# Optimization experiments

Hardware: AMD Instinct MI355X
Metric: run time of the kernel (lower is better)

The kernel has to match this reference:

```python
import jax, jax.numpy as jnp
import numpy as np

N_LOC = 20000
N_EXP = 200000
H = 64
E = 1500000
L = 400000


def setup_inputs() -> dict:
    key = jax.random.key(0)
    ks = jax.random.split(key, 24)
    f = jnp.float32
    w = lambda k, shp: jax.random.normal(k, shp, dtype=f) * 0.1
    # edges: ('location','of','experts'): src in [0,N_LOC), dst in [0,N_EXP)
    src = jax.random.randint(ks[0], (E,), 0, N_LOC)
    dst = jax.random.randint(ks[1], (E,), 0, N_EXP)
    edge_of = jnp.stack([src, dst])          # location -> experts
    edge_rev = jnp.stack([dst, src])         # experts -> location (ToUndirected)
    row = jax.random.randint(ks[2], (L,), 0, N_LOC)
    col = jax.random.randint(ks[3], (L,), 0, N_EXP)
    edge_label_index = jnp.stack([row, col])
    return dict(
        emb_loc=w(ks[4], (N_LOC, H)), emb_exp=w(ks[5], (N_EXP, H)),
        W1l_of=w(ks[6], (H, H)), b1_of=jnp.zeros((H,), f), W1r_of=w(ks[7], (H, H)),
        W1l_rev=w(ks[8], (H, H)), b1_rev=jnp.zeros((H,), f), W1r_rev=w(ks[9], (H, H)),
        W2l_of=w(ks[10], (H, H)), b2_of=jnp.zeros((H,), f), W2r_of=w(ks[11], (H, H)),
        W2l_rev=w(ks[12], (H, H)), b2_rev=jnp.zeros((H,), f), W2r_rev=w(ks[13], (H, H)),
        dW1=w(ks[14], (2 * H, H)), db1=jnp.zeros((H,), f),
        dW2=w(ks[15], (H, 1)), db2=jnp.zeros((1,), f),
        edge_of=edge_of, edge_rev=edge_rev, edge_label_index=edge_label_index,
    )


def _sage(x_src, x_dst, edge, Wl, b, Wr, n_dst):
    # PyG SAGEConv: lin_l(mean of neighbor msgs) + lin_r(x_dst); bias only in lin_l
    s, d = edge[0], edge[1]
    msg = x_src[s]                                   # [E, H] gather
    summed = jax.ops.segment_sum(msg, d, num_segments=n_dst)
    cnt = jax.ops.segment_sum(jnp.ones((edge.shape[1],), x_src.dtype), d, num_segments=n_dst)
    agg = summed / jnp.maximum(cnt, 1.0)[:, None]
    return agg @ Wl + b + x_dst @ Wr


def reference(emb_loc, emb_exp,
              W1l_of, b1_of, W1r_of, W1l_rev, b1_rev, W1r_rev,
              W2l_of, b2_of, W2r_of, W2l_rev, b2_rev, W2r_rev,
              dW1, db1, dW2, db2,
              edge_of, edge_rev, edge_label_index):
    # layer 1 (to_hetero: one conv per edge type; each dst type has one incoming type)
    z_exp = jax.nn.relu(_sage(emb_loc, emb_exp, edge_of, W1l_of, b1_of, W1r_of, N_EXP))
    z_loc = jax.nn.relu(_sage(emb_exp, emb_loc, edge_rev, W1l_rev, b1_rev, W1r_rev, N_LOC))
    # layer 2 (no relu)
    z_exp2 = _sage(z_loc, z_exp, edge_of, W2l_of, b2_of, W2r_of, N_EXP)
    z_loc2 = _sage(z_exp, z_loc, edge_rev, W2l_rev, b2_rev, W2r_rev, N_LOC)
    # EdgeDecoder: gather-concat-MLP
    row, col = edge_label_index[0], edge_label_index[1]
    z = jnp.concatenate([z_loc2[row], z_exp2[col]], axis=-1)  # [L, 2H]
    h = jax.nn.relu(z @ dW1 + db1)
    out = (h @ dW2 + db2).reshape(-1)
    return out
```

## Files before the change

kernel.cpp:

```cpp
#include <hip/hip_runtime.h>

#define H 64
#define NE 1500000
#define NLOC 20000
#define NEXP 200000
#define NL 400000
#define PAD_E 32
#define PAD_L 128
#define EPT 8
#define FILL_CHUNK 2048
#define NCHUNK ((NE + FILL_CHUNK - 1) / FILL_CHUNK)
#define FILL_BLOCKS (NCHUNK * 8)
#define DENSE1_BLOCKS 1280
#define PREP_BLOCKS (5 + DENSE1_BLOCKS + FILL_BLOCKS)

#define WS_NEED 90546112ULL

typedef int vint4 __attribute__((ext_vector_type(4)));
typedef _Float16 f16x8 __attribute__((ext_vector_type(8)));
typedef float f32x4 __attribute__((ext_vector_type(4)));

__device__ __forceinline__ float bcastf(float v, int k) {
  return __int_as_float(__builtin_amdgcn_readlane(__float_as_int(v), k));
}
__device__ __forceinline__ int bcasti(int v, int k) {
  return __builtin_amdgcn_readlane(v, k);
}

__global__ __launch_bounds__(256, 4) void prep_kernel(
    const int* __restrict__ src, const int* __restrict__ dst,
    int* __restrict__ cnt_loc, int* __restrict__ cnt_exp,
    int* __restrict__ nbr_loc, unsigned short* __restrict__ nbr_exp,
    const float* __restrict__ W2r_of, const float* __restrict__ W2l_of,
    const float* __restrict__ W2l_rev, const float* __restrict__ W2r_rev,
    const float* __restrict__ dW1, const float* __restrict__ b2_of,
    const float* __restrict__ b2_rev,
    float* __restrict__ Wf_q, float* __restrict__ Wf_y2,
    float* __restrict__ Wf_t2, float* __restrict__ Wf_p,
    float* __restrict__ bf_q, float* __restrict__ bf_p,
    const float* __restrict__ emb_loc, _Float16* __restrict__ Ylh,
    const float* __restrict__ W1l_of)
{
  const int lane = threadIdx.x & 63;
  if (blockIdx.x < 5) {
    const int w = threadIdx.x >> 6;
    const float* dW1a = dW1;
    const float* dW1b = dW1 + H * H;
    if (blockIdx.x < 4) {
      const float* A; const float* B; float* C;
      switch (blockIdx.x) {
        case 0:  A = W2r_of;  B = dW1b; C = Wf_q;  break;
        case 1:  A = W2l_of;  B = dW1b; C = Wf_y2; break;
        case 2:  A = W2l_rev; B = dW1a; C = Wf_t2; break;
        default: A = W2r_rev; B = dW1a; C = Wf_p;  break;
      }
      float b[H];
#pragma unroll
      for (int k = 0; k < H; k++) b[k] = B[k * H + lane];
      for (int r = w * 16; r < w * 16 + 16; r++) {
        const float xv = A[r * H + lane];
        float a0 = 0.f, a1 = 0.f;
#pragma unroll
        for (int k = 0; k < H; k += 2) {
          a0 += bcastf(xv, k)     * b[k];
          a1 += bcastf(xv, k + 1) * b[k + 1];
        }
        C[r * H + lane] = a0 + a1;
      }
    } else if (w < 2) {
      const float* bv_src = (w == 0) ? b2_of : b2_rev;
      const float* B      = (w == 0) ? dW1b  : dW1a;
      float* o            = (w == 0) ? bf_q  : bf_p;
      float wk[H];
#pragma unroll
      for (int k = 0; k < H; k++) wk[k] = B[k * H + lane];
      const float bv = bv_src[lane];
      float a = 0.f;
#pragma unroll
      for (int k = 0; k < H; k++) a += bcastf(bv, k) * wk[k];
      o[lane] = a;
    }
  } else if (blockIdx.x < 5 + DENSE1_BLOCKS) {
    const int vb = blockIdx.x - 5;
    const int gw = (vb * 256 + threadIdx.x) >> 6;
    const int nw = (DENSE1_BLOCKS * 256) >> 6;
    float w[H];
#pragma unroll
    for (int k = 0; k < H; k++) w[k] = W1l_of[k * H + lane];
    for (int i = gw; i < NLOC; i += nw) {
      const float xv = emb_loc[i * H + lane];
      float a0 = 0.f, a1 = 0.f;
#pragma unroll
      for (int k = 0; k < H; k += 2) {
        a0 += bcastf(xv, k)     * w[k];
        a1 += bcastf(xv, k + 1) * w[k + 1];
      }
      Ylh[i * H + lane] = (_Float16)(a0 + a1);
    }
  } else {
    const int fb = blockIdx.x - (5 + DENSE1_BLOCKS);
    const int p = fb & 7;
    const int chunk = fb >> 3;
    const long base = (long)chunk * FILL_CHUNK + threadIdx.x * EPT;
    if (base >= NE) return;
    vint4 s0 = __builtin_nontemporal_load((const vint4*)(src + base));
    vint4 s1 = __builtin_nontemporal_load((const vint4*)(src + base + 4));
    vint4 d0 = __builtin_nontemporal_load((const vint4*)(dst + base));
    vint4 d1 = __builtin_nontemporal_load((const vint4*)(dst + base + 4));
    int ss[EPT] = {s0.x, s0.y, s0.z, s0.w, s1.x, s1.y, s1.z, s1.w};
    int dd[EPT] = {d0.x, d0.y, d0.z, d0.w, d1.x, d1.y, d1.z, d1.w};
    const int elo = p * (NEXP / 8), ehi = elo + NEXP / 8;
    const int llo = p * (NLOC / 8), lhi = llo + NLOC / 8;
#pragma unroll
    for (int k = 0; k < EPT; k++) {
      const int d = dd[k];
      if (d >= elo && d < ehi) {
        int pos = atomicAdd(&cnt_exp[d], 1);
        if (pos < PAD_E) nbr_exp[d * PAD_E + pos] = (unsigned short)ss[k];
      }
    }
#pragma unroll
    for (int k = 0; k < EPT; k++) {
      const int s = ss[k];
      if (s >= llo && s < lhi) {
        int pos = atomicAdd(&cnt_loc[s], 1);
        if (pos < PAD_L) nbr_loc[s * PAD_L + pos] = dd[k];
      }
    }
  }
}

__global__ __launch_bounds__(256, 4) void mfma_pass_kernel(
    const unsigned short* __restrict__ nbr, const int* __restrict__ cnt,
    const _Float16* __restrict__ y,
    const float* a32, const _Float16* a16,
    _Float16* out1, const float* __restrict__ W1,
    const float* __restrict__ bias, int relu,
    _Float16* out2, const float* __restrict__ W2)
{
  const int w = threadIdx.x >> 6;
  const int lane = threadIdx.x & 63;
  const int q = lane >> 4;
  const int cidx = lane & 15;
  const int rb = blockIdx.x * 16;

  __shared__ float Gs[16 * H];

  f16x8 b1lo, b1hi, b2lo, b2hi;
#pragma unroll
  for (int j = 0; j < 8; j++) {
    b1lo[j] = (_Float16)W1[(q * 8 + j) * H + w * 16 + cidx];
    b1hi[j] = (_Float16)W1[(32 + q * 8 + j) * H + w * 16 + cidx];
  }
  if (out2) {
#pragma unroll
    for (int j = 0; j < 8; j++) {
      b2lo[j] = (_Float16)W2[(q * 8 + j) * H + w * 16 + cidx];
      b2hi[j] = (_Float16)W2[(32 + q * 8 + j) * H + w * 16 + cidx];
    }
  }

  if (y) {
    for (int rr = 0; rr < 4; rr++) {
      const int i = rb + w * 4 + rr;
      const int c = cnt[i];
      const int cc = min(c, PAD_E);
      const unsigned short* nb = nbr + (long)i * PAD_E;
      float s0 = 0.f, s1 = 0.f, s2 = 0.f, s3 = 0.f;
      const int id = (lane < cc) ? (int)nb[lane] : 0;
      int k = 0;
      const int m4 = cc & ~3;
      for (; k < m4; k += 4) {
        const int i0 = bcasti(id, k), i1 = bcasti(id, k + 1),
                  i2 = bcasti(id, k + 2), i3 = bcasti(id, k + 3);
        s0 += (float)y[(long)i0 * H + lane];
        s1 += (float)y[(long)i1 * H + lane];
        s2 += (float)y[(long)i2 * H + lane];
        s3 += (float)y[(long)i3 * H + lane];
      }
      for (; k < cc; k++) s0 += (float)y[(long)bcasti(id, k) * H + lane];
      Gs[(w * 4 + rr) * H + lane] =
          ((s0 + s1) + (s2 + s3)) / fmaxf((float)c, 1.0f);
    }
  }

  f16x8 a0, a1;
  if (a16) {
    const _Float16* ar = a16 + (long)(rb + cidx) * H;
    a0 = *(const f16x8*)(ar + q * 8);
    a1 = *(const f16x8*)(ar + 32 + q * 8);
  } else {
    const float* ar = a32 + (long)(rb + cidx) * H;
#pragma unroll
    for (int j = 0; j < 8; j++) {
      a0[j] = (_Float16)ar[q * 8 + j];
      a1[j] = (_Float16)ar[32 + q * 8 + j];
    }
  }
  f32x4 acc1 = {0.f, 0.f, 0.f, 0.f};
  acc1 = __builtin_amdgcn_mfma_f32_16x16x32_f16(a0, b1lo, acc1, 0, 0, 0);
  acc1 = __builtin_amdgcn_mfma_f32_16x16x32_f16(a1, b1hi, acc1, 0, 0, 0);
  f32x4 acc2 = {0.f, 0.f, 0.f, 0.f};
  if (out2) {
    acc2 = __builtin_amdgcn_mfma_f32_16x16x32_f16(a0, b2lo, acc2, 0, 0, 0);
    acc2 = __builtin_amdgcn_mfma_f32_16x16x32_f16(a1, b2hi, acc2, 0, 0, 0);
  }

  const float bj = bias ? bias[w * 16 + cidx] : 0.f;
  __syncthreads();
#pragma unroll
  for (int reg = 0; reg < 4; reg++) {
    const int r = q * 4 + reg;
    float v = acc1[reg] + bj;
    if (y) v += Gs[r * H + w * 16 + cidx];
    if (relu) v = fmaxf(v, 0.f);
    out1[(long)(rb + r) * H + w * 16 + cidx] = (_Float16)v;
    if (out2)
      out2[(long)(rb + r) * H + w * 16 + cidx] = (_Float16)acc2[reg];
  }
}

__global__ __launch_bounds__(256, 3) void loc_gather_fused_kernel(
    const int* __restrict__ nbr, const int* __restrict__ cnt,
    const _Float16* __restrict__ T, const float* __restrict__ x,
    float* __restrict__ zout, _Float16* __restrict__ y2out,
    const float* __restrict__ Wr, const float* __restrict__ bias,
    const float* __restrict__ Wfy2, int n)
{
  const int lane = threadIdx.x & 63;
  const int gw = (blockIdx.x * 256 + threadIdx.x) >> 6;
  const int nw = (gridDim.x * 256) >> 6;
  float wr[H], wy[H];
#pragma unroll
  for (int k = 0; k < H; k++) {
    wr[k] = Wr[k * H + lane];
    wy[k] = Wfy2[k * H + lane];
  }
  const float bj = bias[lane];
  for (int i = gw; i < n; i += nw) {
    const int c = cnt[i];
    const int cc = min(c, PAD_L);
    const int* nb = nbr + (long)i * PAD_L;
    float s0 = 0.f, s1 = 0.f, s2 = 0.f, s3 = 0.f;
    int e = 0;
    while (e < cc) {
      const int m = min(cc - e, 64);
      const int id = (lane < m) ? nb[e + lane] : 0;
      int k = 0;
      const int m4 = m & ~3;
      for (; k < m4; k += 4) {
        const int i0 = bcasti(id, k), i1 = bcasti(id, k + 1),
                  i2 = bcasti(id, k + 2), i3 = bcasti(id, k + 3);
        s0 += (float)T[(long)i0 * H + lane];
        s1 += (float)T[(long)i1 * H + lane];
        s2 += (float)T[(long)i2 * H + lane];
        s3 += (float)T[(long)i3 * H + lane];
      }
      for (; k < m; k++) s0 += (float)T[(long)bcasti(id, k) * H + lane];
      e += m;
    }
    const float agg = ((s0 + s1) + (s2 + s3)) / fmaxf((float)c, 1.0f);
    const float xv = x[i * H + lane];
    float a0 = 0.f, a1 = 0.f;
#pragma unroll
    for (int k = 0; k < H; k += 2) {
      a0 += bcastf(xv, k)     * wr[k];
      a1 += bcastf(xv, k + 1) * wr[k + 1];
    }
    const float z = fmaxf(agg + bj + a0 + a1, 0.0f);
    zout[i * H + lane] = z;
    float y0 = 0.f, y1 = 0.f;
#pragma unroll
    for (int k = 0; k < H; k += 2) {
      y0 += bcastf(z, k)     * wy[k];
      y1 += bcastf(z, k + 1) * wy[k + 1];
    }
    y2out[i * H + lane] = (_Float16)(y0 + y1);
  }
}

__global__ __launch_bounds__(256, 4) void loc_gather_kernel(
    const int* __restrict__ nbr, const int* __restrict__ cnt,
    const _Float16* __restrict__ T, const float* __restrict__ x,
    _Float16* __restrict__ out16,
    const float* __restrict__ Wr, const float* __restrict__ bias, int n)
{
  const int lane = threadIdx.x & 63;
  const int gw = (blockIdx.x * 256 + threadIdx.x) >> 6;
  const int nw = (gridDim.x * 256) >> 6;
  float wr[H];
#pragma unroll
  for (int k = 0; k < H; k++) wr[k] = Wr[k * H + lane];
  const float bj = bias[lane];
  for (int i = gw; i < n; i += nw) {
    const int c = cnt[i];
    const int cc = min(c, PAD_L);
    const int* nb = nbr + (long)i * PAD_L;
    float s0 = 0.f, s1 = 0.f, s2 = 0.f, s3 = 0.f;
    int e = 0;
    while (e < cc) {
      const int m = min(cc - e, 64);
      const int id = (lane < m) ? nb[e + lane] : 0;
      int k = 0;
      const int m4 = m & ~3;
      for (; k < m4; k += 4) {
        const int i0 = bcasti(id, k), i1 = bcasti(id, k + 1),
                  i2 = bcasti(id, k + 2), i3 = bcasti(id, k + 3);
        s0 += (float)T[(long)i0 * H + lane];
        s1 += (float)T[(long)i1 * H + lane];
        s2 += (float)T[(long)i2 * H + lane];
        s3 += (float)T[(long)i3 * H + lane];
      }
      for (; k < m; k++) s0 += (float)T[(long)bcasti(id, k) * H + lane];
      e += m;
    }
    const float agg = ((s0 + s1) + (s2 + s3)) / fmaxf((float)c, 1.0f);
    const float xv = x[i * H + lane];
    float a0 = 0.f, a1 = 0.f;
#pragma unroll
    for (int k = 0; k < H; k += 2) {
      a0 += bcastf(xv, k)     * wr[k];
      a1 += bcastf(xv, k + 1) * wr[k + 1];
    }
    out16[i * H + lane] = (_Float16)(agg + bj + a0 + a1);
  }
}

__global__ __launch_bounds__(256, 4) void edge_kernel(
    const int* __restrict__ row, const int* __restrict__ col,
    const _Float16* __restrict__ P, const _Float16* __restrict__ Q,
    const float* __restrict__ db1, const float* __restrict__ dW2,
    const float* __restrict__ db2, float* __restrict__ out)
{
  const int lane = threadIdx.x & 63;
  const int gw = (blockIdx.x * 256 + threadIdx.x) >> 6;
  const int nw = (gridDim.x * 256) >> 6;
  const float bj = db1[lane];
  const float w2 = dW2[lane];
  const float b2 = db2[0];
  for (int e = gw * 4; e < NL; e += nw * 4) {
    const int n4 = min(NL - e, 4);
    float h[4];
#pragma unroll
    for (int k = 0; k < 4; k++) {
      if (k < n4) {
        const int r = row[e + k], c = col[e + k];
        const float p = (float)P[(long)r * H + lane];
        const float q = (float)Q[(long)c * H + lane];
        h[k] = fmaxf(p + q + bj, 0.0f) * w2;
      } else h[k] = 0.f;
    }
#pragma unroll
    for (int off = 1; off < 64; off <<= 1) {
#pragma unroll
      for (int k = 0; k < 4; k++) h[k] += __shfl_xor(h[k], off);
    }
    if (lane == 0) {
#pragma unroll
      for (int k = 0; k < 4; k++)
        if (k < n4) out[e + k] = h[k] + b2;
    }
  }
}

extern "C" void kernel_launch(void* const* d_in, const int* in_sizes, int n_in,
                              void* d_out, int out_size, void* d_ws, size_t ws_size,
                              hipStream_t stream) {
  const float* emb_loc = (const float*)d_in[0];
  const float* emb_exp = (const float*)d_in[1];
  const float* W1l_of  = (const float*)d_in[2];
  const float* b1_of   = (const float*)d_in[3];
  const float* W1r_of  = (const float*)d_in[4];
  const float* W1l_rev = (const float*)d_in[5];
  const float* b1_rev  = (const float*)d_in[6];
  const float* W1r_rev = (const float*)d_in[7];
  const float* W2l_of  = (const float*)d_in[8];
  const float* b2_of   = (const float*)d_in[9];
  const float* W2r_of  = (const float*)d_in[10];
  const float* W2l_rev = (const float*)d_in[11];
  const float* b2_rev  = (const float*)d_in[12];
  const float* W2r_rev = (const float*)d_in[13];
  const float* dW1     = (const float*)d_in[14];
  const float* db1     = (const float*)d_in[15];
  const float* dW2     = (const float*)d_in[16];
  const float* db2     = (const float*)d_in[17];
  const int*   edge_of = (const int*)d_in[18];
  const int*   eli     = (const int*)d_in[20];

  const int* src = edge_of;
  const int* dst = edge_of + NE;
  const int* row = eli;
  const int* col = eli + NL;

  if (ws_size < WS_NEED) return;

  char* ws = (char*)d_ws;
  int*            cnt_loc = (int*)(ws);
  int*            cnt_exp = (int*)(ws + 80000);
  int*            nbr_loc = (int*)(ws + 880064);
  unsigned short* nbr_exp = (unsigned short*)(ws + 11120064);
  _Float16*       Ylh     = (_Float16*)(ws + 23920064);
  _Float16*       Y2fh    = (_Float16*)(ws + 26480064);
  float*          z_loc   = (float*)(ws + 29040064);
  _Float16*       PH      = (_Float16*)(ws + 34160064);
  _Float16*       ZE      = (_Float16*)(ws + 39280064);
  _Float16*       TH      = (_Float16*)(ws + 64880064);
  float*          Wf_q    = (float*)(ws + 90480064);
  float*          Wf_y2   = (float*)(ws + 90496448);
  float*          Wf_t2   = (float*)(ws + 90512832);
  float*          Wf_p    = (float*)(ws + 90529216);
  float*          bf_q    = (float*)(ws + 90545600);
  float*          bf_p    = (float*)(ws + 90545856);
  float*          out     = (float*)d_out;

  (void)hipMemsetAsync(ws, 0, 880000, stream);
  prep_kernel<<<PREP_BLOCKS, 256, 0, stream>>>(
      src, dst, cnt_loc, cnt_exp, nbr_loc, nbr_exp,
      W2r_of, W2l_of, W2l_rev, W2r_rev, dW1, b2_of, b2_rev,
      Wf_q, Wf_y2, Wf_t2, Wf_p, bf_q, bf_p,
      emb_loc, Ylh, W1l_of);

  mfma_pass_kernel<<<NEXP / 16, 256, 0, stream>>>(nbr_exp, cnt_exp, Ylh,
      emb_exp, (const _Float16*)nullptr, ZE, W1r_of, b1_of, 1, TH, W1l_rev);

  loc_gather_fused_kernel<<<1250, 256, 0, stream>>>(nbr_loc, cnt_loc, TH,
      emb_loc, z_loc, Y2fh, W1r_rev, b1_rev, Wf_y2, NLOC);

  mfma_pass_kernel<<<NEXP / 16, 256, 0, stream>>>(nbr_exp, cnt_exp, Y2fh,
      (const float*)nullptr, ZE, ZE, Wf_q, bf_q, 0, TH, Wf_t2);

  loc_gather_kernel<<<1250, 256, 0, stream>>>(nbr_loc, cnt_loc, TH,
      z_loc, PH, Wf_p, bf_p, NLOC);

  edge_kernel<<<2048, 256, 0, stream>>>(row, col, PH, ZE,
                                        db1, dW2, db2, out);
}
```

Measured before the change: 613.8 us.

## Restructure passes: compute z_exp projections in first pass, merge final gathers

The first expert pass now computes the relu'd z_exp tile, stages it in shared memory, and immediately applies the folded Wf_q and Wf_t2 projections. This removes the need to store and reread ZE in a second dense pass. The second expert pass becomes a gather-only update of PQ, and it is merged with the location gather into one launch using a block-range split. Folded weights now live in the output buffer as scratch, since edge_kernel overwrites it later, and the first pass uses more registers with launch bounds lowered to 3.

```diff
diff --git a/kernel.cpp b/kernel.cpp
--- a/kernel.cpp
+++ b/kernel.cpp
@@ -13,8 +13,10 @@
 #define FILL_BLOCKS (NCHUNK * 8)
 #define DENSE1_BLOCKS 1280
 #define PREP_BLOCKS (5 + DENSE1_BLOCKS + FILL_BLOCKS)
-
-#define WS_NEED 90546112ULL
+#define QFIN_BLOCKS 4096
+#define LOC2_BLOCKS 1250
+
+#define WS_NEED 113520000ULL
 
 typedef int vint4 __attribute__((ext_vector_type(4)));
 typedef _Float16 f16x8 __attribute__((ext_vector_type(8)));
@@ -34,10 +36,7 @@
     const float* __restrict__ W2r_of, const float* __restrict__ W2l_of,
     const float* __restrict__ W2l_rev, const float* __restrict__ W2r_rev,
     const float* __restrict__ dW1, const float* __restrict__ b2_of,
-    const float* __restrict__ b2_rev,
-    float* __restrict__ Wf_q, float* __restrict__ Wf_y2,
-    float* __restrict__ Wf_t2, float* __restrict__ Wf_p,
-    float* __restrict__ bf_q, float* __restrict__ bf_p,
+    const float* __restrict__ b2_rev, float* __restrict__ fold,
     const float* __restrict__ emb_loc, _Float16* __restrict__ Ylh,
     const float* __restrict__ W1l_of)
 {
@@ -49,10 +48,10 @@
     if (blockIdx.x < 4) {
       const float* A; const float* B; float* C;
       switch (blockIdx.x) {
-        case 0:  A = W2r_of;  B = dW1b; C = Wf_q;  break;
-        case 1:  A = W2l_of;  B = dW1b; C = Wf_y2; break;
-        case 2:  A = W2l_rev; B = dW1a; C = Wf_t2; break;
-        default: A = W2r_rev; B = dW1a; C = Wf_p;  break;
+        case 0:  A = W2r_of;  B = dW1b; C = fold;         break;
+        case 1:  A = W2l_of;  B = dW1b; C = fold + 4096;  break;
+        case 2:  A = W2l_rev; B = dW1a; C = fold + 8192;  break;
+        default: A = W2r_rev; B = dW1a; C = fold + 12288; break;
       }
       float b[H];
 #pragma unroll
@@ -70,7 +69,7 @@
     } else if (w < 2) {
       const float* bv_src = (w == 0) ? b2_of : b2_rev;
       const float* B      = (w == 0) ? dW1b  : dW1a;
-      float* o            = (w == 0) ? bf_q  : bf_p;
+      float* o            = (w == 0) ? fold + 16384 : fold + 16448;
       float wk[H];
 #pragma unroll
       for (int k = 0; k < H; k++) wk[k] = B[k * H + lane];
@@ -130,93 +129,106 @@
   }
 }
 
-__global__ __launch_bounds__(256, 4) void mfma_pass_kernel(
+__global__ __launch_bounds__(256, 3) void passA_kernel(
     const unsigned short* __restrict__ nbr, const int* __restrict__ cnt,
-    const _Float16* __restrict__ y,
-    const float* a32, const _Float16* a16,
-    _Float16* out1, const float* __restrict__ W1,
-    const float* __restrict__ bias, int relu,
-    _Float16* out2, const float* __restrict__ W2)
+    const _Float16* __restrict__ y, const float* __restrict__ x,
+    const float* __restrict__ W1r_of, const float* __restrict__ b1_of,
+    const float* __restrict__ W1l_rev,
+    const float* __restrict__ Wf_q, const float* __restrict__ Wf_t2,
+    _Float16* __restrict__ T1h, _Float16* __restrict__ PQ,
+    _Float16* __restrict__ T2h)
 {
   const int w = threadIdx.x >> 6;
   const int lane = threadIdx.x & 63;
   const int q = lane >> 4;
   const int cidx = lane & 15;
   const int rb = blockIdx.x * 16;
+  const int col = w * 16 + cidx;
 
   __shared__ float Gs[16 * H];
-
-  f16x8 b1lo, b1hi, b2lo, b2hi;
+  __shared__ float Zs[16][H + 1];
+
+  f16x8 bz0, bz1, bt0, bt1;
 #pragma unroll
   for (int j = 0; j < 8; j++) {
-    b1lo[j] = (_Float16)W1[(q * 8 + j) * H + w * 16 + cidx];
-    b1hi[j] = (_Float16)W1[(32 + q * 8 + j) * H + w * 16 + cidx];
-  }
-  if (out2) {
-#pragma unroll
-    for (int j = 0; j < 8; j++) {
-      b2lo[j] = (_Float16)W2[(q * 8 + j) * H + w * 16 + cidx];
-      b2hi[j] = (_Float16)W2[(32 + q * 8 + j) * H + w * 16 + cidx];
-    }
-  }
-
-  if (y) {
-    for (int rr = 0; rr < 4; rr++) {
-      const int i = rb + w * 4 + rr;
-      const int c = cnt[i];
-      const int cc = min(c, PAD_E);
-      const unsigned short* nb = nbr + (long)i * PAD_E;
-      float s0 = 0.f, s1 = 0.f, s2 = 0.f, s3 = 0.f;
-      const int id = (lane < cc) ? (int)nb[lane] : 0;
-      int k = 0;
-      const int m4 = cc & ~3;
-      for (; k < m4; k += 4) {
-        const int i0 = bcasti(id, k), i1 = bcasti(id, k + 1),
-                  i2 = bcasti(id, k + 2), i3 = bcasti(id, k + 3);
-        s0 += (float)y[(long)i0 * H + lane];
-        s1 += (float)y[(long)i1 * H + lane];
-        s2 += (float)y[(long)i2 * H + lane];
-        s3 += (float)y[(long)i3 * H + lane];
-      }
-      for (; k < cc; k++) s0 += (float)y[(long)bcasti(id, k) * H + lane];
-      Gs[(w * 4 + rr) * H + lane] =
-          ((s0 + s1) + (s2 + s3)) / fmaxf((float)c, 1.0f);
-    }
-  }
-
+    bz0[j] = (_Float16)W1r_of[(q * 8 + j) * H + col];
+    bz1[j] = (_Float16)W1r_of[(32 + q * 8 + j) * H + col];
+    bt0[j] = (_Float16)W1l_rev[(q * 8 + j) * H + col];
+    bt1[j] = (_Float16)W1l_rev[(32 + q * 8 + j) * H + col];
+  }
+
+  for (int rr = 0; rr < 4; rr++) {
+    const int i = rb + w * 4 + rr;
+    const int c = cnt[i];
+    const int cc = min(c, PAD_E);
+    const unsigned short* nb = nbr + (long)i * PAD_E;
+    float s0 = 0.f, s1 = 0.f, s2 = 0.f, s3 = 0.f;
+    const int id = (lane < cc) ? (int)nb[lane] : 0;
+    int k = 0;
+    const int m4 = cc & ~3;
+    for (; k < m4; k += 4) {
+      const int i0 = bcasti(id, k), i1 = bcasti(id, k + 1),
+                i2 = bcasti(id, k + 2), i3 = bcasti(id, k + 3);
+      s0 += (float)y[(long)i0 * H + lane];
+      s1 += (float)y[(long)i1 * H + lane];
+      s2 += (float)y[(long)i2 * H + lane];
+      s3 += (float)y[(long)i3 * H + lane];
+    }
+    for (; k < cc; k++) s0 += (float)y[(long)bcasti(id, k) * H + lane];
+    Gs[(w * 4 + rr) * H + lane] =
+        ((s0 + s1) + (s2 + s3)) / fmaxf((float)c, 1.0f);
+  }
+
+  const float* ar = x + (long)(rb + cidx) * H;
   f16x8 a0, a1;
-  if (a16) {
-    const _Float16* ar = a16 + (long)(rb + cidx) * H;
-    a0 = *(const f16x8*)(ar + q * 8);
-    a1 = *(const f16x8*)(ar + 32 + q * 8);
-  } else {
-    const float* ar = a32 + (long)(rb + cidx) * H;
-#pragma unroll
-    for (int j = 0; j < 8; j++) {
-      a0[j] = (_Float16)ar[q * 8 + j];
-      a1[j] = (_Float16)ar[32 + q * 8 + j];
-    }
-  }
-  f32x4 acc1 = {0.f, 0.f, 0.f, 0.f};
-  acc1 = __builtin_amdgcn_mfma_f32_16x16x32_f16(a0, b1lo, acc1, 0, 0, 0);
-  acc1 = __builtin_amdgcn_mfma_f32_16x16x32_f16(a1, b1hi, acc1, 0, 0, 0);
-  f32x4 acc2 = {0.f, 0.f, 0.f, 0.f};
-  if (out2) {
-    acc2 = __builtin_amdgcn_mfma_f32_16x16x32_f16(a0, b2lo, acc2, 0, 0, 0);
-    acc2 = __builtin_amdgcn_mfma_f32_16x16x32_f16(a1, b2hi, acc2, 0, 0, 0);
-  }
-
-  const float bj = bias ? bias[w * 16 + cidx] : 0.f;
+#pragma unroll
+  for (int j = 0; j < 8; j++) {
+    a0[j] = (_Float16)ar[q * 8 + j];
+    a1[j] = (_Float16)ar[32 + q * 8 + j];
+  }
+  f32x4 accz = {0.f, 0.f, 0.f, 0.f};
+  accz = __builtin_amdgcn_mfma_f32_16x16x32_f16(a0, bz0, accz, 0, 0, 0);
+  accz = __builtin_amdgcn_mfma_f32_16x16x32_f16(a1, bz1, accz, 0, 0, 0);
+  f32x4 acct = {0.f, 0.f, 0.f, 0.f};
+  acct = __builtin_amdgcn_mfma_f32_16x16x32_f16(a0, bt0, acct, 0, 0, 0);
+  acct = __builtin_amdgcn_mfma_f32_16x16x32_f16(a1, bt1, acct, 0, 0, 0);
+
+  const float bj = b1_of[col];
   __syncthreads();
 #pragma unroll
   for (int reg = 0; reg < 4; reg++) {
     const int r = q * 4 + reg;
-    float v = acc1[reg] + bj;
-    if (y) v += Gs[r * H + w * 16 + cidx];
-    if (relu) v = fmaxf(v, 0.f);
-    out1[(long)(rb + r) * H + w * 16 + cidx] = (_Float16)v;
-    if (out2)
-      out2[(long)(rb + r) * H + w * 16 + cidx] = (_Float16)acc2[reg];
+    const float z = fmaxf(accz[reg] + Gs[r * H + col] + bj, 0.f);
+    Zs[r][col] = z;
+    T1h[(long)(rb + r) * H + col] = (_Float16)acct[reg];
+  }
+
+  f16x8 bq0, bq1, b20, b21;
+#pragma unroll
+  for (int j = 0; j < 8; j++) {
+    bq0[j] = (_Float16)Wf_q[(q * 8 + j) * H + col];
+    bq1[j] = (_Float16)Wf_q[(32 + q * 8 + j) * H + col];
+    b20[j] = (_Float16)Wf_t2[(q * 8 + j) * H + col];
+    b21[j] = (_Float16)Wf_t2[(32 + q * 8 + j) * H + col];
+  }
+  __syncthreads();
+  f16x8 az0, az1;
+#pragma unroll
+  for (int j = 0; j < 8; j++) {
+    az0[j] = (_Float16)Zs[cidx][q * 8 + j];
+    az1[j] = (_Float16)Zs[cidx][32 + q * 8 + j];
+  }
+  f32x4 accq = {0.f, 0.f, 0.f, 0.f};
+  accq = __builtin_amdgcn_mfma_f32_16x16x32_f16(az0, bq0, accq, 0, 0, 0);
+  accq = __builtin_amdgcn_mfma_f32_16x16x32_f16(az1, bq1, accq, 0, 0, 0);
+  f32x4 acc2 = {0.f, 0.f, 0.f, 0.f};
+  acc2 = __builtin_amdgcn_mfma_f32_16x16x32_f16(az0, b20, acc2, 0, 0, 0);
+  acc2 = __builtin_amdgcn_mfma_f32_16x16x32_f16(az1, b21, acc2, 0, 0, 0);
+#pragma unroll
+  for (int reg = 0; reg < 4; reg++) {
+    const int r = q * 4 + reg;
+    PQ[(long)(rb + r) * H + col]  = (_Float16)accq[reg];
+    T2h[(long)(rb + r) * H + col] = (_Float16)acc2[reg];
   }
 }
 
@@ -279,50 +291,81 @@
   }
 }
 
-__global__ __launch_bounds__(256, 4) void loc_gather_kernel(
-    const int* __restrict__ nbr, const int* __restrict__ cnt,
-    const _Float16* __restrict__ T, const float* __restrict__ x,
-    _Float16* __restrict__ out16,
-    const float* __restrict__ Wr, const float* __restrict__ bias, int n)
+__global__ __launch_bounds__(256, 4) void fin_kernel(
+    const unsigned short* __restrict__ nbr_e, const int* __restrict__ cnt_e,
+    const _Float16* __restrict__ Y2fh, _Float16* __restrict__ PQ,
+    const float* __restrict__ bf_q,
+    const int* __restrict__ nbr_l, const int* __restrict__ cnt_l,
+    const _Float16* __restrict__ T2h, const float* __restrict__ z_loc,
+    _Float16* __restrict__ PH, const float* __restrict__ Wf_p,
+    const float* __restrict__ bf_p)
 {
   const int lane = threadIdx.x & 63;
-  const int gw = (blockIdx.x * 256 + threadIdx.x) >> 6;
-  const int nw = (gridDim.x * 256) >> 6;
-  float wr[H];
-#pragma unroll
-  for (int k = 0; k < H; k++) wr[k] = Wr[k * H + lane];
-  const float bj = bias[lane];
-  for (int i = gw; i < n; i += nw) {
-    const int c = cnt[i];
-    const int cc = min(c, PAD_L);
-    const int* nb = nbr + (long)i * PAD_L;
-    float s0 = 0.f, s1 = 0.f, s2 = 0.f, s3 = 0.f;
-    int e = 0;
-    while (e < cc) {
-      const int m = min(cc - e, 64);
-      const int id = (lane < m) ? nb[e + lane] : 0;
+  if (blockIdx.x < QFIN_BLOCKS) {
+    const int gw = (blockIdx.x * 256 + threadIdx.x) >> 6;
+    const int nw = (QFIN_BLOCKS * 256) >> 6;
+    const float bq = bf_q[lane];
+    for (int i = gw; i < NEXP; i += nw) {
+      const int c = cnt_e[i];
+      const int cc = min(c, PAD_E);
+      const unsigned short* nb = nbr_e + (long)i * PAD_E;
+      float s0 = 0.f, s1 = 0.f, s2 = 0.f, s3 = 0.f;
+      const int id = (lane < cc) ? (int)nb[lane] : 0;
       int k = 0;
-      const int m4 = m & ~3;
+      const int m4 = cc & ~3;
       for (; k < m4; k += 4) {
         const int i0 = bcasti(id, k), i1 = bcasti(id, k + 1),
                   i2 = bcasti(id, k + 2), i3 = bcasti(id, k + 3);
-        s0 += (float)T[(long)i0 * H + lane];
-        s1 += (float)T[(long)i1 * H + lane];
-        s2 += (float)T[(long)i2 * H + lane];
-        s3 += (float)T[(long)i3 * H + lane];
-      }
-      for (; k < m; k++) s0 += (float)T[(long)bcasti(id, k) * H + lane];
-      e += m;
-    }
-    const float agg = ((s0 + s1) + (s2 + s3)) / fmaxf((float)c, 1.0f);
-    const float xv = x[i * H + lane];
-    float a0 = 0.f, a1 = 0.f;
-#pragma unroll
-    for (int k = 0; k < H; k += 2) {
-      a0 += bcastf(xv, k)     * wr[k];
-      a1 += bcastf(xv, k + 1) * wr[k + 1];
-    }
-    out16[i * H + lane] = (_Float16)(agg + bj + a0 + a1);
+        s0 += (float)Y2fh[(long)i0 * H + lane];
+        s1 += (float)Y2fh[(long)i1 * H + lane];
+        s2 += (float)Y2fh[(long)i2 * H + lane];
+        s3 += (float)Y2fh[(long)i3 * H + lane];
+      }
+      for (; k < cc; k++) s0 += (float)Y2fh[(long)bcasti(id, k) * H + lane];
+      const float agg = ((s0 + s1) + (s2 + s3)) / fmaxf((float)c, 1.0f);
+      PQ[(long)i * H + lane] =
+          (_Float16)((float)PQ[(long)i * H + lane] + agg + bq);
+    }
+  } else {
+    const int vb = blockIdx.x - QFIN_BLOCKS;
+    const int gw = (vb * 256 + threadIdx.x) >> 6;
+    const int nw = (LOC2_BLOCKS * 256) >> 6;
+    float wr[H];
+#pragma unroll
+    for (int k = 0; k < H; k++) wr[k] = Wf_p[k * H + lane];
+    const float bj = bf_p[lane];
+    for (int i = gw; i < NLOC; i += nw) {
+      const int c = cnt_l[i];
+      const int cc = min(c, PAD_L);
+      const int* nb = nbr_l + (long)i * PAD_L;
+      float s0 = 0.f, s1 = 0.f, s2 = 0.f, s3 = 0.f;
+      int e = 0;
+      while (e < cc) {
+        const int m = min(cc - e, 64);
+        const int id = (lane < m) ? nb[e + lane] : 0;
+        int k = 0;
+        const int m4 = m & ~3;
+        for (; k < m4; k += 4) {
+          const int i0 = bcasti(id, k), i1 = bcasti(id, k + 1),
+                    i2 = bcasti(id, k + 2), i3 = bcasti(id, k + 3);
+          s0 += (float)T2h[(long)i0 * H + lane];
+          s1 += (float)T2h[(long)i1 * H + lane];
+          s2 += (float)T2h[(long)i2 * H + lane];
+          s3 += (float)T2h[(long)i3 * H + lane];
+        }
+        for (; k < m; k++) s0 += (float)T2h[(long)bcasti(id, k) * H + lane];
+        e += m;
+      }
+      const float agg = ((s0 + s1) + (s2 + s3)) / fmaxf((float)c, 1.0f);
+      const float xv = z_loc[i * H + lane];
+      float a0 = 0.f, a1 = 0.f;
+#pragma unroll
+      for (int k = 0; k < H; k += 2) {
+        a0 += bcastf(xv, k)     * wr[k];
+        a1 += bcastf(xv, k + 1) * wr[k + 1];
+      }
+      PH[i * H + lane] = (_Float16)(agg + bj + a0 + a1);
+    }
   }
 }
 
@@ -397,41 +440,41 @@
   char* ws = (char*)d_ws;
   int*            cnt_loc = (int*)(ws);
   int*            cnt_exp = (int*)(ws + 80000);
-  int*            nbr_loc = (int*)(ws + 880064);
-  unsigned short* nbr_exp = (unsigned short*)(ws + 11120064);
-  _Float16*       Ylh     = (_Float16*)(ws + 23920064);
-  _Float16*       Y2fh    = (_Float16*)(ws + 26480064);
-  float*          z_loc   = (float*)(ws + 29040064);
-  _Float16*       PH      = (_Float16*)(ws + 34160064);
-  _Float16*       ZE      = (_Float16*)(ws + 39280064);
-  _Float16*       TH      = (_Float16*)(ws + 64880064);
-  float*          Wf_q    = (float*)(ws + 90480064);
-  float*          Wf_y2   = (float*)(ws + 90496448);
-  float*          Wf_t2   = (float*)(ws + 90512832);
-  float*          Wf_p    = (float*)(ws + 90529216);
-  float*          bf_q    = (float*)(ws + 90545600);
-  float*          bf_p    = (float*)(ws + 90545856);
+  int*            nbr_loc = (int*)(ws + 880000);
+  unsigned short* nbr_exp = (unsigned short*)(ws + 11120000);
+  _Float16*       Ylh     = (_Float16*)(ws + 23920000);
+  _Float16*       Y2fh    = (_Float16*)(ws + 26480000);
+  float*          z_loc   = (float*)(ws + 29040000);
+  _Float16*       PH      = (_Float16*)(ws + 34160000);
+  _Float16*       PQ      = (_Float16*)(ws + 36720000);
+  _Float16*       T1h     = (_Float16*)(ws + 62320000);
+  _Float16*       T2h     = (_Float16*)(ws + 87920000);
   float*          out     = (float*)d_out;
+
+  float* fold  = (float*)d_out;
+  float* Wf_q  = fold;
+  float* Wf_y2 = fold + 4096;
+  float* Wf_t2 = fold + 8192;
+  float* Wf_p  = fold + 12288;
+  float* bf_q  = fold + 16384;
+  float* bf_p  = fold + 16448;
 
   (void)hipMemsetAsync(ws, 0, 880000, stream);
   prep_kernel<<<PREP_BLOCKS, 256, 0, stream>>>(
       src, dst, cnt_loc, cnt_exp, nbr_loc, nbr_exp,
-      W2r_of, W2l_of, W2l_rev, W2r_rev, dW1, b2_of, b2_rev,
-      Wf_q, Wf_y2, Wf_t2, Wf_p, bf_q, bf_p,
+      W2r_of, W2l_of, W2l_rev, W2r_rev, dW1, b2_of, b2_rev, fold,
       emb_loc, Ylh, W1l_of);
 
-  mfma_pass_kernel<<<NEXP / 16, 256, 0, stream>>>(nbr_exp, cnt_exp, Ylh,
-      emb_exp, (const _Float16*)nullptr, ZE, W1r_of, b1_of, 1, TH, W1l_rev);
-
-  loc_gather_fused_kernel<<<1250, 256, 0, stream>>>(nbr_loc, cnt_loc, TH,
+  passA_kernel<<<NEXP / 16, 256, 0, stream>>>(nbr_exp, cnt_exp, Ylh, emb_exp,
+      W1r_of, b1_of, W1l_rev, Wf_q, Wf_t2, T1h, PQ, T2h);
+
+  loc_gather_fused_kernel<<<1250, 256, 0, stream>>>(nbr_loc, cnt_loc, T1h,
       emb_loc, z_loc, Y2fh, W1r_rev, b1_rev, Wf_y2, NLOC);
 
-  mfma_pass_kernel<<<NEXP / 16, 256, 0, stream>>>(nbr_exp, cnt_exp, Y2fh,
-      (const float*)nullptr, ZE, ZE, Wf_q, bf_q, 0, TH, Wf_t2);
-
-  loc_gather_kernel<<<1250, 256, 0, stream>>>(nbr_loc, cnt_loc, TH,
-      z_loc, PH, Wf_p, bf_p, NLOC);
-
-  edge_kernel<<<2048, 256, 0, stream>>>(row, col, PH, ZE,
+  fin_kernel<<<QFIN_BLOCKS + LOC2_BLOCKS, 256, 0, stream>>>(
+      nbr_exp, cnt_exp, Y2fh, PQ, bf_q,
+      nbr_loc, cnt_loc, T2h, z_loc, PH, Wf_p, bf_p);
+
+  edge_kernel<<<2048, 256, 0, stream>>>(row, col, PH, PQ,
                                         db1, dW2, db2, out);
 }
```

Measured after the change: 645.2 us. 5.1% more time.
